# Kernel optimization log

Hardware: AMD Instinct MI355X
Metric: run time of the kernel (lower is better)

The kernel has to match this reference:

```python
import jax, jax.numpy as jnp
import numpy as np

B, S, D = 2, 1024, 4096
H, HD = 32, 128
ROPE_THETA = 10000.0
QMAX = 127.0  # int8 symmetric


def fake_quant_int8(x):
    # per-tensor symmetric int8 quantize-dequantize
    scale = jnp.maximum(jnp.max(jnp.abs(x)), 1e-8) / QMAX
    q = jnp.clip(jnp.round(x / scale), -QMAX, QMAX) * scale
    # straight-through estimator (matches typical fake-quant autograd)
    return x + jax.lax.stop_gradient(q - x)


def rope_cos_sin(position_ids, head_dim, dtype):
    inv_freq = 1.0 / (ROPE_THETA ** (jnp.arange(0, head_dim, 2, dtype=jnp.float32) / head_dim))
    freqs = position_ids.astype(jnp.float32)[..., None] * inv_freq[None, None, :]  # [B,S,hd/2]
    emb = jnp.concatenate([freqs, freqs], axis=-1)  # [B,S,hd]
    return jnp.cos(emb).astype(dtype), jnp.sin(emb).astype(dtype)


def rotate_half(x):
    x1, x2 = jnp.split(x, 2, axis=-1)
    return jnp.concatenate([-x2, x1], axis=-1)


def setup_inputs() -> dict:
    key = jax.random.key(0)
    ks = jax.random.split(key, 6)
    inv = 1.0 / np.sqrt(D)
    return {
        'hidden_states': jax.random.normal(ks[0], (B, S, D), jnp.float32),
        'wq': jax.random.normal(ks[1], (D, D), jnp.float32) * inv,
        'wk': jax.random.normal(ks[2], (D, D), jnp.float32) * inv,
        'wv': jax.random.normal(ks[3], (D, D), jnp.float32) * inv,
        'wo': jax.random.normal(ks[4], (D, D), jnp.float32) * inv,
        'position_ids': jnp.broadcast_to(jnp.arange(S, dtype=jnp.int32)[None, :], (B, S)),
    }


def reference(hidden_states, wq, wk, wv, wo, position_ids):
    bsz, q_len, _ = hidden_states.shape
    # QKV projections (F.linear: x @ W.T, weight layout [out, in])
    q = jnp.einsum('bsd,ed->bse', hidden_states, wq).reshape(bsz, q_len, H, HD).transpose(0, 2, 1, 3)
    k = jnp.einsum('bsd,ed->bse', hidden_states, wk).reshape(bsz, q_len, H, HD).transpose(0, 2, 1, 3)
    v = jnp.einsum('bsd,ed->bse', hidden_states, wv).reshape(bsz, q_len, H, HD).transpose(0, 2, 1, 3)

    cos, sin = rope_cos_sin(position_ids, HD, q.dtype)  # [B,S,HD]
    cos, sin = cos[:, None, :, :], sin[:, None, :, :]
    q = q * cos + rotate_half(q) * sin
    k = k * cos + rotate_half(k) * sin

    # inline fake-quant on K, Q
    k = fake_quant_int8(k)
    q = fake_quant_int8(q)

    attn_weights = jnp.einsum('bhqd,bhkd->bhqk', q, k) / jnp.sqrt(jnp.asarray(HD, q.dtype))
    attn_weights = fake_quant_int8(attn_weights)  # s_quantizer

    # causal additive mask
    causal = jnp.tril(jnp.ones((q_len, q_len), dtype=bool))
    attn_weights = jnp.where(causal[None, None], attn_weights, jnp.asarray(-1e9, attn_weights.dtype))

    probs = jax.nn.softmax(attn_weights.astype(jnp.float32), axis=-1).astype(q.dtype)
    probs = fake_quant_int8(probs)   # p_quantizer
    v = fake_quant_int8(v)           # v_quantizer (per-tensor => transpose is a no-op)

    attn_out = jnp.einsum('bhqk,bhkd->bhqd', probs, v)
    attn_out = fake_quant_int8(attn_out)  # o_quantizer

    attn_out = attn_out.transpose(0, 2, 1, 3).reshape(bsz, q_len, D)
    return jnp.einsum('bsd,ed->bse', attn_out, wo)
```

## Files before the change

### kernel.cpp

```cpp
#include <hip/hip_runtime.h>
#include <cstdint>
#include <cstddef>

#define DEVI __device__ __forceinline__

typedef __attribute__((ext_vector_type(8))) short short8;
typedef __attribute__((ext_vector_type(4))) float f32x4;

static constexpr int kS = 1024, kH = 32;
static constexpr int kM = 2048;
static constexpr float kInvSqrtHD = 0.08838834764831845f;
static constexpr float kMaskVal = -3.0e38f;

static constexpr size_t OFF_A    = 0;
static constexpr size_t A_HSB    = 0;
static constexpr size_t A_WQKV   = 16777216;
static constexpr size_t A_QQ     = 0;
static constexpr size_t A_KQ     = 16777216;
static constexpr size_t A_VT     = 33554432;
static constexpr size_t A_AO     = 50331648;
static constexpr size_t A_AOB    = 83886080;
static constexpr size_t OFF_QKV  = 117440512;
static constexpr size_t OFF_TAB  = 167772160;
static constexpr size_t OFF_RED  = 168296448;

DEVI unsigned short f2bf(float x) {
  unsigned u = __float_as_uint(x);
  return (unsigned short)((u + 0x7FFFu + ((u >> 16) & 1u)) >> 16);
}
DEVI float bf2f(short u) { return __uint_as_float(((unsigned)(unsigned short)u) << 16); }

DEVI void gload_lds16(const void* g, void* l) {
  __builtin_amdgcn_global_load_lds((const __attribute__((address_space(1))) unsigned int*)g,
                                   (__attribute__((address_space(3))) unsigned int*)l,
                                   16, 0, 0);
}
DEVI f32x4 mfma16(short8 a, short8 b, f32x4 c) {
  return __builtin_amdgcn_mfma_f32_16x16x32_bf16(a, b, c, 0, 0, 0);
}
DEVI float wave_max(float v) {
  #pragma unroll
  for (int o = 32; o; o >>= 1) v = fmaxf(v, __shfl_xor(v, o));
  return v;
}
DEVI float wave_sum(float v) {
  #pragma unroll
  for (int o = 32; o; o >>= 1) v += __shfl_xor(v, o);
  return v;
}
DEVI float clamp127(float x) { return fminf(fmaxf(x, -127.0f), 127.0f); }

__global__ __launch_bounds__(256) void convert_hqkv(
    const float* __restrict__ hs, const float* __restrict__ wq,
    const float* __restrict__ wk, const float* __restrict__ wv,
    unsigned short* __restrict__ hs_b, unsigned short* __restrict__ wqkv_b)
{
  const size_t NHS = 8388608ULL, WN = 16777216ULL;
  const size_t n4 = (NHS + 3 * WN) / 4;
  for (size_t i4 = (size_t)blockIdx.x * 256 + threadIdx.x; i4 < n4;
       i4 += (size_t)gridDim.x * 256) {
    size_t i = i4 * 4;
    const float* src; unsigned short* dst;
    if (i < NHS) { src = hs + i; dst = hs_b + i; }
    else {
      size_t j = i - NHS;
      src = (j < WN) ? (wq + j) : (j < 2 * WN) ? (wk + (j - WN)) : (wv + (j - 2 * WN));
      dst = wqkv_b + j;
    }
    float4 v = *(const float4*)src;
    unsigned long long p =
        (unsigned long long)f2bf(v.x) | ((unsigned long long)f2bf(v.y) << 16) |
        ((unsigned long long)f2bf(v.z) << 32) | ((unsigned long long)f2bf(v.w) << 48);
    *(unsigned long long*)dst = p;
  }
}

__global__ __launch_bounds__(256) void convert_wo(
    const float* __restrict__ wo, unsigned short* __restrict__ wo_b)
{
  const size_t n4 = 16777216ULL / 4;
  for (size_t i4 = (size_t)blockIdx.x * 256 + threadIdx.x; i4 < n4;
       i4 += (size_t)gridDim.x * 256) {
    size_t i = i4 * 4;
    float4 v = *(const float4*)(wo + i);
    unsigned long long p =
        (unsigned long long)f2bf(v.x) | ((unsigned long long)f2bf(v.y) << 16) |
        ((unsigned long long)f2bf(v.z) << 32) | ((unsigned long long)f2bf(v.w) << 48);
    *(unsigned long long*)(wo_b + i) = p;
  }
}

__global__ void rope_table(float* __restrict__ ct, float* __restrict__ st) {
  int i = blockIdx.x * blockDim.x + threadIdx.x;
  if (i >= kS * 64) return;
  int s = i >> 6, j = i & 63;
  float invf = 1.0f / powf(10000.0f, (float)j / 64.0f);
  float fr = (float)s * invf;
  ct[i] = cosf(fr);
  st[i] = sinf(fr);
}

template <int OUTBF>
__global__ __launch_bounds__(256) void gemm_nt(
    const unsigned short* __restrict__ A, const unsigned short* __restrict__ Bt,
    void* __restrict__ Cv, int M, int N, int K,
    const unsigned* __restrict__ red, int redidx)
{
  __shared__ __align__(16) unsigned short As[128 * 64];
  __shared__ __align__(16) unsigned short Bs[128 * 64];
  const int tid = threadIdx.x, l = tid & 63, w = tid >> 6;
  const int m0 = blockIdx.y * 128, n0 = blockIdx.x * 128;
  const int wr = w >> 1, wc = w & 1;
  const int lrow = l >> 3, lsl = l & 7;
  const int srcks = lsl ^ lrow;
  f32x4 acc[4][4];
  #pragma unroll
  for (int a = 0; a < 4; ++a)
    #pragma unroll
    for (int b = 0; b < 4; ++b) { acc[a][b][0] = 0.f; acc[a][b][1] = 0.f; acc[a][b][2] = 0.f; acc[a][b][3] = 0.f; }

  for (int k0 = 0; k0 < K; k0 += 64) {
    #pragma unroll
    for (int j = 0; j < 4; ++j) {
      int c = w * 4 + j;
      int row = c * 8 + lrow;
      gload_lds16(A  + (size_t)(m0 + row) * K + k0 + srcks * 8, (char*)As + c * 1024);
      gload_lds16(Bt + (size_t)(n0 + row) * K + k0 + srcks * 8, (char*)Bs + c * 1024);
    }
    __syncthreads();
    #pragma unroll
    for (int kk = 0; kk < 2; ++kk) {
      short8 af[4], bf[4];
      #pragma unroll
      for (int mi = 0; mi < 4; ++mi) {
        int row = wr * 64 + mi * 16 + (l & 15);
        int slot = (kk * 4 + (l >> 4)) ^ (row & 7);
        af[mi] = *(const short8*)((const char*)As + row * 128 + slot * 16);
      }
      #pragma unroll
      for (int ni = 0; ni < 4; ++ni) {
        int row = wc * 64 + ni * 16 + (l & 15);
        int slot = (kk * 4 + (l >> 4)) ^ (row & 7);
        bf[ni] = *(const short8*)((const char*)Bs + row * 128 + slot * 16);
      }
      #pragma unroll
      for (int mi = 0; mi < 4; ++mi)
        #pragma unroll
        for (int ni = 0; ni < 4; ++ni)
          acc[mi][ni] = mfma16(af[mi], bf[ni], acc[mi][ni]);
    }
    __syncthreads();
  }

  float alpha = 1.0f;
  if (redidx >= 0) alpha = fmaxf(__uint_as_float(red[redidx]), 1e-8f) / 127.0f;
  #pragma unroll
  for (int mi = 0; mi < 4; ++mi) {
    int row = m0 + wr * 64 + mi * 16 + (l >> 4) * 4;
    #pragma unroll
    for (int ni = 0; ni < 4; ++ni) {
      int col = n0 + wc * 64 + ni * 16 + (l & 15);
      #pragma unroll
      for (int i = 0; i < 4; ++i) {
        float v = acc[mi][ni][i] * alpha;
        if constexpr (OUTBF) ((unsigned short*)Cv)[(size_t)(row + i) * N + col] = f2bf(v);
        else                 ((float*)Cv)[(size_t)(row + i) * N + col] = v;
      }
    }
  }
}

__global__ __launch_bounds__(256) void rope_absmax(
    const unsigned short* __restrict__ qkv, const int* __restrict__ pos,
    const float* __restrict__ ct, const float* __restrict__ st,
    unsigned* __restrict__ red)
{
  int t = threadIdx.x;
  int h = t >> 3, jc = (t & 7) * 8;
  float mq = 0.f, mk = 0.f, mv = 0.f;
  for (int bs = blockIdx.x; bs < kM; bs += gridDim.x) {
    int p = pos[bs];
    const unsigned short* row = qkv + (size_t)bs * 12288;
    float cs[8], sn[8];
    #pragma unroll
    for (int e = 0; e < 8; ++e) { cs[e] = ct[p * 64 + jc + e]; sn[e] = st[p * 64 + jc + e]; }
    {
      short8 x1 = *(const short8*)(row + h * 128 + jc);
      short8 x2 = *(const short8*)(row + h * 128 + 64 + jc);
      #pragma unroll
      for (int e = 0; e < 8; ++e) {
        float a = bf2f(x1[e]), b = bf2f(x2[e]);
        mq = fmaxf(mq, fmaxf(fabsf(a * cs[e] - b * sn[e]), fabsf(b * cs[e] + a * sn[e])));
      }
    }
    {
      short8 x1 = *(const short8*)(row + 4096 + h * 128 + jc);
      short8 x2 = *(const short8*)(row + 4096 + h * 128 + 64 + jc);
      #pragma unroll
      for (int e = 0; e < 8; ++e) {
        float a = bf2f(x1[e]), b = bf2f(x2[e]);
        mk = fmaxf(mk, fmaxf(fabsf(a * cs[e] - b * sn[e]), fabsf(b * cs[e] + a * sn[e])));
      }
    }
    {
      short8 v0 = *(const short8*)(row + 8192 + t * 16);
      short8 v1 = *(const short8*)(row + 8192 + t * 16 + 8);
      #pragma unroll
      for (int e = 0; e < 8; ++e) mv = fmaxf(mv, fmaxf(fabsf(bf2f(v0[e])), fabsf(bf2f(v1[e]))));
    }
  }
  mq = wave_max(mq); mk = wave_max(mk); mv = wave_max(mv);
  __shared__ float sm[3][4];
  int w = t >> 6;
  if ((t & 63) == 0) { sm[0][w] = mq; sm[1][w] = mk; sm[2][w] = mv; }
  __syncthreads();
  if (t == 0) {
    atomicMax(red + 0, __float_as_uint(fmaxf(fmaxf(sm[0][0], sm[0][1]), fmaxf(sm[0][2], sm[0][3]))));
    atomicMax(red + 1, __float_as_uint(fmaxf(fmaxf(sm[1][0], sm[1][1]), fmaxf(sm[1][2], sm[1][3]))));
    atomicMax(red + 2, __float_as_uint(fmaxf(fmaxf(sm[2][0], sm[2][1]), fmaxf(sm[2][2], sm[2][3]))));
  }
}

__global__ __launch_bounds__(256) void quant_qk_rope(
    const unsigned short* __restrict__ qkv, const int* __restrict__ pos,
    const float* __restrict__ ct, const float* __restrict__ st,
    const unsigned* __restrict__ red,
    unsigned short* __restrict__ qq, unsigned short* __restrict__ kq)
{
  int bs = blockIdx.x, t = threadIdx.x;
  int b = bs >> 10, s = bs & 1023;
  int p = pos[bs];
  float iq = 127.0f / fmaxf(__uint_as_float(red[0]), 1e-8f);
  float ik = 127.0f / fmaxf(__uint_as_float(red[1]), 1e-8f);
  const unsigned short* row = qkv + (size_t)bs * 12288;
  int h = t >> 3, jc = (t & 7) * 8;
  float cs[8], sn[8];
  #pragma unroll
  for (int e = 0; e < 8; ++e) { cs[e] = ct[p * 64 + jc + e]; sn[e] = st[p * 64 + jc + e]; }
  size_t ob = ((size_t)(b * kH + h) * kS + s) * 128;
  {
    short8 x1 = *(const short8*)(row + h * 128 + jc);
    short8 x2 = *(const short8*)(row + h * 128 + 64 + jc);
    short8 o1, o2;
    #pragma unroll
    for (int e = 0; e < 8; ++e) {
      float a = bf2f(x1[e]), b2 = bf2f(x2[e]);
      o1[e] = (short)f2bf(clamp127(rintf((a * cs[e] - b2 * sn[e]) * iq)));
      o2[e] = (short)f2bf(clamp127(rintf((b2 * cs[e] + a * sn[e]) * iq)));
    }
    *(short8*)(qq + ob + jc) = o1;
    *(short8*)(qq + ob + 64 + jc) = o2;
  }
  {
    short8 x1 = *(const short8*)(row + 4096 + h * 128 + jc);
    short8 x2 = *(const short8*)(row + 4096 + h * 128 + 64 + jc);
    short8 o1, o2;
    #pragma unroll
    for (int e = 0; e < 8; ++e) {
      float a = bf2f(x1[e]), b2 = bf2f(x2[e]);
      o1[e] = (short)f2bf(clamp127(rintf((a * cs[e] - b2 * sn[e]) * ik)));
      o2[e] = (short)f2bf(clamp127(rintf((b2 * cs[e] + a * sn[e]) * ik)));
    }
    *(short8*)(kq + ob + jc) = o1;
    *(short8*)(kq + ob + 64 + jc) = o2;
  }
}

__global__ __launch_bounds__(256) void quantT_v(
    const unsigned short* __restrict__ qkv, const unsigned* __restrict__ red,
    unsigned short* __restrict__ vt)
{
  __shared__ float tile[32][132];
  int bh = blockIdx.x, st0 = blockIdx.y * 32;
  int b = bh >> 5, h = bh & 31;
  float iv = 127.0f / fmaxf(__uint_as_float(red[2]), 1e-8f);
  int t = threadIdx.x;
  #pragma unroll
  for (int e = 0; e < 2; ++e) {
    int idx = (e * 256 + t) * 8;
    int sl = idx >> 7, hd = idx & 127;
    short8 xv = *(const short8*)(qkv + (size_t)(b * 1024 + st0 + sl) * 12288 + 8192 + h * 128 + hd);
    #pragma unroll
    for (int q = 0; q < 8; ++q) tile[sl][hd + q] = clamp127(rintf(bf2f(xv[q]) * iv));
  }
  __syncthreads();
  #pragma unroll
  for (int e = 0; e < 16; ++e) {
    int idx = e * 256 + t;
    int sl = idx & 31, hd = idx >> 5;
    vt[((size_t)bh * 128 + hd) * kS + st0 + sl] = f2bf(tile[sl][hd]);
  }
}

__global__ __launch_bounds__(256) void qk_absmax_gemm(
    const unsigned short* __restrict__ qq, const unsigned short* __restrict__ kq,
    unsigned* __restrict__ red)
{
  __shared__ __align__(16) unsigned short As[128 * 64];
  __shared__ __align__(16) unsigned short Bs[128 * 64];
  const int tid = threadIdx.x, l = tid & 63, w = tid >> 6;
  const int bh = blockIdx.z;
  const int m0 = blockIdx.y * 128, n0 = blockIdx.x * 128;
  const unsigned short* A  = qq + (size_t)bh * 131072;
  const unsigned short* Bt = kq + (size_t)bh * 131072;
  const int wr = w >> 1, wc = w & 1;
  const int lrow = l >> 3, lsl = l & 7;
  const int srcks = lsl ^ lrow;
  f32x4 acc[4][4];
  #pragma unroll
  for (int a = 0; a < 4; ++a)
    #pragma unroll
    for (int b = 0; b < 4; ++b) { acc[a][b][0] = 0.f; acc[a][b][1] = 0.f; acc[a][b][2] = 0.f; acc[a][b][3] = 0.f; }

  for (int k0 = 0; k0 < 128; k0 += 64) {
    #pragma unroll
    for (int j = 0; j < 4; ++j) {
      int c = w * 4 + j;
      int row = c * 8 + lrow;
      gload_lds16(A  + (size_t)(m0 + row) * 128 + k0 + srcks * 8, (char*)As + c * 1024);
      gload_lds16(Bt + (size_t)(n0 + row) * 128 + k0 + srcks * 8, (char*)Bs + c * 1024);
    }
    __syncthreads();
    #pragma unroll
    for (int kk = 0; kk < 2; ++kk) {
      short8 af[4], bf[4];
      #pragma unroll
      for (int mi = 0; mi < 4; ++mi) {
        int row = wr * 64 + mi * 16 + (l & 15);
        int slot = (kk * 4 + (l >> 4)) ^ (row & 7);
        af[mi] = *(const short8*)((const char*)As + row * 128 + slot * 16);
      }
      #pragma unroll
      for (int ni = 0; ni < 4; ++ni) {
        int row = wc * 64 + ni * 16 + (l & 15);
        int slot = (kk * 4 + (l >> 4)) ^ (row & 7);
        bf[ni] = *(const short8*)((const char*)Bs + row * 128 + slot * 16);
      }
      #pragma unroll
      for (int mi = 0; mi < 4; ++mi)
        #pragma unroll
        for (int ni = 0; ni < 4; ++ni)
          acc[mi][ni] = mfma16(af[mi], bf[ni], acc[mi][ni]);
    }
    __syncthreads();
  }

  float vmax = 0.f;
  #pragma unroll
  for (int mi = 0; mi < 4; ++mi)
    #pragma unroll
    for (int ni = 0; ni < 4; ++ni)
      #pragma unroll
      for (int i = 0; i < 4; ++i) vmax = fmaxf(vmax, fabsf(acc[mi][ni][i]));
  vmax = wave_max(vmax);
  __shared__ float sm[4];
  if (l == 0) sm[w] = vmax;
  __syncthreads();
  if (tid == 0)
    atomicMax(red + 3, __float_as_uint(fmaxf(fmaxf(sm[0], sm[1]), fmaxf(sm[2], sm[3]))));
}

__global__ __launch_bounds__(256) void softmax_pv(
    const unsigned short* __restrict__ qq, const unsigned short* __restrict__ kq,
    const unsigned short* __restrict__ vt,
    unsigned* __restrict__ red, float* __restrict__ ao)
{
  __shared__ unsigned short Lg[16][1024];
  int bh = blockIdx.x, r0 = blockIdx.y * 16;
  int t = threadIdx.x, l = t & 63, w = t >> 6;
  float sq = fmaxf(__uint_as_float(red[0]), 1e-8f) / 127.0f;
  float sk = fmaxf(__uint_as_float(red[1]), 1e-8f) / 127.0f;
  const float c1 = sq * sk * kInvSqrtHD;
  float sl = fmaxf(__uint_as_float(red[3]) * c1, 1e-8f) / 127.0f;
  float isl = 1.0f / sl;
  const unsigned short* qb = qq + (size_t)bh * 131072;
  const unsigned short* kb = kq + (size_t)bh * 131072;
  const unsigned short* vb = vt + (size_t)bh * 131072;
  const int ktop = r0 >> 4;
  const int blimit = r0 + 16;

  short8 aq[4];
  #pragma unroll
  for (int s = 0; s < 4; ++s)
    aq[s] = *(const short8*)(qb + (size_t)(r0 + (l & 15)) * 128 + s * 32 + (l >> 4) * 8);
  for (int kt = w; kt <= ktop; kt += 4) {
    int key0 = kt * 16;
    short8 bq[4];
    #pragma unroll
    for (int s = 0; s < 4; ++s)
      bq[s] = *(const short8*)(kb + (size_t)(key0 + (l & 15)) * 128 + s * 32 + (l >> 4) * 8);
    f32x4 acc; acc[0] = 0.f; acc[1] = 0.f; acc[2] = 0.f; acc[3] = 0.f;
    #pragma unroll
    for (int s = 0; s < 4; ++s) acc = mfma16(aq[s], bq[s], acc);
    int col = key0 + (l & 15);
    #pragma unroll
    for (int i = 0; i < 4; ++i) {
      int rl = (l >> 4) * 4 + i;
      float qv = (col > r0 + rl) ? kMaskVal : clamp127(rintf(acc[i] * c1 * isl));
      Lg[rl][col ^ ((rl & 7) << 3)] = f2bf(qv);
    }
  }
  __syncthreads();

  const int nch = (blimit + 511) >> 9;
  #pragma unroll
  for (int r = 0; r < 4; ++r) {
    int row = w * 4 + r, xm = (row & 7) << 3;
    float vals[2][8];
    float m = kMaskVal;
    for (int j = 0; j < nch; ++j) {
      int base = j * 512 + l * 8;
      short8 v = *(const short8*)&Lg[row][base ^ xm];
      #pragma unroll
      for (int e = 0; e < 8; ++e) {
        float f = (base + e < blimit) ? bf2f(v[e]) : kMaskVal;
        vals[j][e] = f;
        m = fmaxf(m, f);
      }
    }
    m = wave_max(m);
    float sum = 0.f;
    float ex[2][8];
    for (int j = 0; j < nch; ++j)
      #pragma unroll
      for (int e = 0; e < 8; ++e) { ex[j][e] = __expf((vals[j][e] - m) * sl); sum += ex[j][e]; }
    sum = wave_sum(sum);
    float inv127 = 127.0f / sum;
    for (int j = 0; j < nch; ++j) {
      int base = j * 512 + l * 8;
      short8 o;
      #pragma unroll
      for (int e = 0; e < 8; ++e) o[e] = (short)f2bf(rintf(ex[j][e] * inv127));
      *(short8*)&Lg[row][base ^ xm] = o;
    }
  }
  __syncthreads();

  float sv = fmaxf(__uint_as_float(red[2]), 1e-8f) / 127.0f;
  const float c2 = sv * (1.0f / 127.0f);
  const int ksmax = (r0 + 47) >> 5;
  f32x4 pacc[2];
  pacc[0][0]=0.f;pacc[0][1]=0.f;pacc[0][2]=0.f;pacc[0][3]=0.f;
  pacc[1][0]=0.f;pacc[1][1]=0.f;pacc[1][2]=0.f;pacc[1][3]=0.f;
  for (int ks = 0; ks < ksmax; ++ks) {
    int r = l & 15, c0 = ks * 32 + (l >> 4) * 8;
    short8 af = *(const short8*)&Lg[r][c0 ^ ((r & 7) << 3)];
    #pragma unroll
    for (int j = 0; j < 2; ++j) {
      int hd = (w * 2 + j) * 16 + (l & 15);
      short8 bf = *(const short8*)(vb + (size_t)hd * kS + ks * 32 + (l >> 4) * 8);
      pacc[j] = mfma16(af, bf, pacc[j]);
    }
  }
  float vmax = 0.f;
  #pragma unroll
  for (int j = 0; j < 2; ++j) {
    int hd = (w * 2 + j) * 16 + (l & 15);
    int rbase = r0 + (l >> 4) * 4;
    #pragma unroll
    for (int i = 0; i < 4; ++i) {
      float val = pacc[j][i] * c2;
      ao[((size_t)bh * kS + rbase + i) * 128 + hd] = val;
      vmax = fmaxf(vmax, fabsf(val));
    }
  }
  vmax = wave_max(vmax);
  __shared__ float sm2[4];
  if (l == 0) sm2[w] = vmax;
  __syncthreads();
  if (t == 0)
    atomicMax(red + 4, __float_as_uint(fmaxf(fmaxf(sm2[0], sm2[1]), fmaxf(sm2[2], sm2[3]))));
}

__global__ __launch_bounds__(256) void quant_ao(
    const float* __restrict__ ao, const unsigned* __restrict__ red,
    unsigned short* __restrict__ aob)
{
  float ia = 127.0f / fmaxf(__uint_as_float(red[4]), 1e-8f);
  const int n = 64 * kS * 128;
  for (int i = blockIdx.x * 256 + threadIdx.x; i < n; i += gridDim.x * 256) {
    int bh = i >> 17, rem = i & 131071;
    int s = rem >> 7, hd = rem & 127;
    int b = bh >> 5, h = bh & 31;
    aob[((size_t)(b * 1024 + s)) * 4096 + h * 128 + hd] = f2bf(clamp127(rintf(ao[i] * ia)));
  }
}

extern "C" void kernel_launch(void* const* d_in, const int* in_sizes, int n_in,
                              void* d_out, int out_size, void* d_ws, size_t ws_size,
                              hipStream_t stream) {
  const float* hs = (const float*)d_in[0];
  const float* wq = (const float*)d_in[1];
  const float* wk = (const float*)d_in[2];
  const float* wv = (const float*)d_in[3];
  const float* wo = (const float*)d_in[4];
  const int* pos  = (const int*)d_in[5];
  char* ws = (char*)d_ws;

  unsigned short* hs_b   = (unsigned short*)(ws + OFF_A + A_HSB);
  unsigned short* wqkv_b = (unsigned short*)(ws + OFF_A + A_WQKV);
  unsigned short* qq     = (unsigned short*)(ws + OFF_A + A_QQ);
  unsigned short* kq     = (unsigned short*)(ws + OFF_A + A_KQ);
  unsigned short* vt     = (unsigned short*)(ws + OFF_A + A_VT);
  float*          ao     = (float*)(ws + OFF_A + A_AO);
  unsigned short* aob    = (unsigned short*)(ws + OFF_A + A_AOB);
  unsigned short* qkv    = (unsigned short*)(ws + OFF_QKV);
  unsigned short* wo_b   = (unsigned short*)(ws + OFF_QKV);
  float*          rc     = (float*)(ws + OFF_TAB);
  float*          rs     = (float*)(ws + OFF_TAB + 262144);
  unsigned*       red    = (unsigned*)(ws + OFF_RED);

  (void)hipMemsetAsync(red, 0, 256, stream);

  rope_table<<<dim3(256), dim3(256), 0, stream>>>(rc, rs);
  convert_hqkv<<<dim3(2048), dim3(256), 0, stream>>>(hs, wq, wk, wv, hs_b, wqkv_b);
  gemm_nt<1><<<dim3(96, 16), dim3(256), 0, stream>>>(hs_b, wqkv_b, qkv, kM, 12288, 4096, red, -1);
  rope_absmax<<<dim3(256), dim3(256), 0, stream>>>(qkv, pos, rc, rs, red);
  quant_qk_rope<<<dim3(2048), dim3(256), 0, stream>>>(qkv, pos, rc, rs, red, qq, kq);
  quantT_v<<<dim3(64, 32), dim3(256), 0, stream>>>(qkv, red, vt);
  convert_wo<<<dim3(1024), dim3(256), 0, stream>>>(wo, wo_b);
  qk_absmax_gemm<<<dim3(8, 8, 64), dim3(256), 0, stream>>>(qq, kq, red);
  softmax_pv<<<dim3(64, 64), dim3(256), 0, stream>>>(qq, kq, vt, red, ao);
  quant_ao<<<dim3(2048), dim3(256), 0, stream>>>(ao, red, aob);
  gemm_nt<0><<<dim3(32, 16), dim3(256), 0, stream>>>(aob, wo_b, d_out, kM, 4096, 4096, red, 4);
}
```

Before: 830.2 us.

## Use 256x256-tile 8-wave pipelined GEMM for fused QKV projection

Adds a new bf16 MFMA GEMM kernel with 256x256 output tiles, 512 threads (8 waves) and double-buffered LDS staged directly from global memory in 32-wide K halves. Loads for the next K step are interleaved with MFMA phases, using s_setprio and explicit waitcnt/barriers. The QKV projection now uses it in place of the 128x128 kernel. The aim is more data reuse per loaded byte and hiding global load latency. The cost is higher register and LDS use and a grid of only 384 blocks, which may leave some CUs idle.

```diff
diff --git a/kernel.cpp b/kernel.cpp
--- a/kernel.cpp
+++ b/kernel.cpp
@@ -98,6 +98,152 @@
   float fr = (float)s * invf;
   ct[i] = cosf(fr);
   st[i] = sinf(fr);
+}
+
+DEVI void stage_half256(const unsigned short* __restrict__ Mat, int rowbase, int K,
+                        int kcol, unsigned short* lbase, int w, int l)
+{
+  int c = 2 * w;
+  int r = c * 16 + (l >> 2);
+  int s = ((l & 3) ^ ((r >> 1) & 3)) * 8;
+  gload_lds16(Mat + (size_t)(rowbase + r) * K + kcol + s, lbase + c * 512);
+  int r2 = r + 16;
+  gload_lds16(Mat + (size_t)(rowbase + r2) * K + kcol + s, lbase + (c + 1) * 512);
+}
+
+DEVI short8 frag256(const unsigned short* khbuf, int r, int l) {
+  int ss = (l >> 4) ^ ((r >> 1) & 3);
+  return *(const short8*)(khbuf + r * 32 + ss * 8);
+}
+
+template <int OUTBF>
+__global__ __launch_bounds__(512, 2) void gemm_nt8(
+    const unsigned short* __restrict__ A, const unsigned short* __restrict__ Bt,
+    void* __restrict__ Cv, int M, int N, int K,
+    const unsigned* __restrict__ red, int redidx)
+{
+  __shared__ __align__(16) unsigned short L[2][2][2][256 * 32];
+  const int tid = threadIdx.x, l = tid & 63, w = tid >> 6;
+  const int wr = w >> 2, wc = w & 3;
+  const int m0 = blockIdx.y * 256, n0 = blockIdx.x * 256;
+  const int NT = K >> 6;
+
+  f32x4 acc[8][4];
+  #pragma unroll
+  for (int x = 0; x < 8; ++x)
+    #pragma unroll
+    for (int y = 0; y < 4; ++y) { acc[x][y][0]=0.f; acc[x][y][1]=0.f; acc[x][y][2]=0.f; acc[x][y][3]=0.f; }
+
+  stage_half256(A,  m0, K, 0,  &L[0][0][0][0], w, l);
+  stage_half256(Bt, n0, K, 0,  &L[0][1][0][0], w, l);
+  stage_half256(A,  m0, K, 32, &L[0][0][1][0], w, l);
+  stage_half256(Bt, n0, K, 32, &L[0][1][1][0], w, l);
+  asm volatile("s_waitcnt vmcnt(4)" ::: "memory");
+  __builtin_amdgcn_s_barrier();
+
+  int d = 0;
+  for (int t = 0; t < NT; ++t) {
+    const int last = (t == NT - 1);
+    const int nd = d ^ 1;
+    const int k1 = (t + 1) << 6;
+    short8 a[4], b[4];
+
+    {
+      const unsigned short* Ab = &L[d][0][0][0];
+      const unsigned short* Bb = &L[d][1][0][0];
+      #pragma unroll
+      for (int i = 0; i < 4; ++i) a[i] = frag256(Ab, wr * 128 + i * 16 + (l & 15), l);
+      #pragma unroll
+      for (int i = 0; i < 4; ++i) b[i] = frag256(Bb, wc * 64 + i * 16 + (l & 15), l);
+    }
+    if (!last) stage_half256(A, m0, K, k1, &L[nd][0][0][0], w, l);
+    __builtin_amdgcn_s_barrier();
+    asm volatile("s_waitcnt lgkmcnt(0)" ::: "memory");
+    __builtin_amdgcn_sched_barrier(0);
+    __builtin_amdgcn_s_setprio(1);
+    #pragma unroll
+    for (int i = 0; i < 4; ++i)
+      #pragma unroll
+      for (int j = 0; j < 4; ++j) acc[i][j] = mfma16(a[i], b[j], acc[i][j]);
+    __builtin_amdgcn_s_setprio(0);
+    __builtin_amdgcn_s_barrier();
+
+    {
+      const unsigned short* Ab = &L[d][0][0][0];
+      #pragma unroll
+      for (int i = 0; i < 4; ++i) a[i] = frag256(Ab, wr * 128 + (4 + i) * 16 + (l & 15), l);
+    }
+    if (!last) stage_half256(Bt, n0, K, k1, &L[nd][1][0][0], w, l);
+    __builtin_amdgcn_s_barrier();
+    asm volatile("s_waitcnt lgkmcnt(0)" ::: "memory");
+    __builtin_amdgcn_sched_barrier(0);
+    __builtin_amdgcn_s_setprio(1);
+    #pragma unroll
+    for (int i = 0; i < 4; ++i)
+      #pragma unroll
+      for (int j = 0; j < 4; ++j) acc[4 + i][j] = mfma16(a[i], b[j], acc[4 + i][j]);
+    __builtin_amdgcn_s_setprio(0);
+    if (!last) asm volatile("s_waitcnt vmcnt(4)" ::: "memory");
+    else       asm volatile("s_waitcnt vmcnt(0)" ::: "memory");
+    __builtin_amdgcn_s_barrier();
+
+    {
+      const unsigned short* Ab = &L[d][0][1][0];
+      const unsigned short* Bb = &L[d][1][1][0];
+      #pragma unroll
+      for (int i = 0; i < 4; ++i) a[i] = frag256(Ab, wr * 128 + i * 16 + (l & 15), l);
+      #pragma unroll
+      for (int i = 0; i < 4; ++i) b[i] = frag256(Bb, wc * 64 + i * 16 + (l & 15), l);
+    }
+    if (!last) stage_half256(A, m0, K, k1 + 32, &L[nd][0][1][0], w, l);
+    __builtin_amdgcn_s_barrier();
+    asm volatile("s_waitcnt lgkmcnt(0)" ::: "memory");
+    __builtin_amdgcn_sched_barrier(0);
+    __builtin_amdgcn_s_setprio(1);
+    #pragma unroll
+    for (int i = 0; i < 4; ++i)
+      #pragma unroll
+      for (int j = 0; j < 4; ++j) acc[i][j] = mfma16(a[i], b[j], acc[i][j]);
+    __builtin_amdgcn_s_setprio(0);
+    __builtin_amdgcn_s_barrier();
+
+    {
+      const unsigned short* Ab = &L[d][0][1][0];
+      #pragma unroll
+      for (int i = 0; i < 4; ++i) a[i] = frag256(Ab, wr * 128 + (4 + i) * 16 + (l & 15), l);
+    }
+    if (!last) stage_half256(Bt, n0, K, k1 + 32, &L[nd][1][1][0], w, l);
+    __builtin_amdgcn_s_barrier();
+    asm volatile("s_waitcnt lgkmcnt(0)" ::: "memory");
+    __builtin_amdgcn_sched_barrier(0);
+    __builtin_amdgcn_s_setprio(1);
+    #pragma unroll
+    for (int i = 0; i < 4; ++i)
+      #pragma unroll
+      for (int j = 0; j < 4; ++j) acc[4 + i][j] = mfma16(a[i], b[j], acc[4 + i][j]);
+    __builtin_amdgcn_s_setprio(0);
+    if (!last) asm volatile("s_waitcnt vmcnt(4)" ::: "memory");
+    __builtin_amdgcn_s_barrier();
+
+    d = nd;
+  }
+
+  float alpha = 1.0f;
+  if (redidx >= 0) alpha = fmaxf(__uint_as_float(red[redidx]), 1e-8f) / 127.0f;
+  #pragma unroll
+  for (int mi = 0; mi < 8; ++mi) {
+    int row = m0 + wr * 128 + mi * 16 + (l >> 4) * 4;
+    #pragma unroll
+    for (int ni = 0; ni < 4; ++ni) {
+      int col = n0 + wc * 64 + ni * 16 + (l & 15);
+      #pragma unroll
+      for (int i = 0; i < 4; ++i) {
+        float v = acc[mi][ni][i] * alpha;
+        if constexpr (OUTBF) ((unsigned short*)Cv)[(size_t)(row + i) * N + col] = f2bf(v);
+        else                 ((float*)Cv)[(size_t)(row + i) * N + col] = v;
+      }
+    }
+  }
 }
 
 template <int OUTBF>
@@ -514,7 +660,7 @@
 
   rope_table<<<dim3(256), dim3(256), 0, stream>>>(rc, rs);
   convert_hqkv<<<dim3(2048), dim3(256), 0, stream>>>(hs, wq, wk, wv, hs_b, wqkv_b);
-  gemm_nt<1><<<dim3(96, 16), dim3(256), 0, stream>>>(hs_b, wqkv_b, qkv, kM, 12288, 4096, red, -1);
+  gemm_nt8<1><<<dim3(48, 8), dim3(512), 0, stream>>>(hs_b, wqkv_b, qkv, kM, 12288, 4096, red, -1);
   rope_absmax<<<dim3(256), dim3(256), 0, stream>>>(qkv, pos, rc, rs, red);
   quant_qk_rope<<<dim3(2048), dim3(256), 0, stream>>>(qkv, pos, rc, rs, red, qq, kq);
   quantT_v<<<dim3(64, 32), dim3(256), 0, stream>>>(qkv, red, vt);
```

New measurement: 811.9 us. 1.02x faster.
